# Optimization experiments

Measured on AMD Instinct MI355X. Metric: run time of the kernel, lower is better.

## Reference

```python
import jax, jax.numpy as jnp
import numpy as np

D_MODEL = 512
N_HEAD = 8
D_HEAD = D_MODEL // N_HEAD
EPS = 1e-6


def setup_inputs() -> dict:
    key = jax.random.key(0)
    ks = jax.random.split(key, 11)
    b, s, d = 4, 8192, D_MODEL
    scale = 1.0 / np.sqrt(d)
    inp = {
        "q": jax.random.normal(ks[0], (b, s, d), jnp.float32),
        "k": jax.random.normal(ks[1], (b, s, d), jnp.float32),
        "v": jax.random.normal(ks[2], (b, s, d), jnp.float32),
        "Wq": jax.random.normal(ks[3], (d, d), jnp.float32) * scale,
        "bq": jax.random.normal(ks[4], (d,), jnp.float32) * 0.01,
        "Wk": jax.random.normal(ks[5], (d, d), jnp.float32) * scale,
        "bk": jax.random.normal(ks[6], (d,), jnp.float32) * 0.01,
        "Wv": jax.random.normal(ks[7], (d, d), jnp.float32) * scale,
        "bv": jax.random.normal(ks[8], (d,), jnp.float32) * 0.01,
        "Wo": jax.random.normal(ks[9], (d, d), jnp.float32) * scale,
        "bo": jax.random.normal(ks[10], (d,), jnp.float32) * 0.01,
    }
    return inp


def reference(q, k, v, Wq, bq, Wk, bk, Wv, bv, Wo, bo):
    b, s, d = q.shape
    # torch nn.Linear: x @ W.T + b
    feat = lambda x, W, bias: jax.nn.elu(
        (x @ W.T + bias).reshape(b, s, N_HEAD, D_HEAD)) + 1.0
    queries = feat(q, Wq, bq)                      # [b,s,h,dh]
    keys = feat(k, Wk, bk)                         # [b,s,h,dh]
    values = (v @ Wv.T + bv).reshape(b, s, N_HEAD, D_HEAD)
    # full-sequence KV summary state
    k_v = jnp.einsum('bshd,bshm->bhdm', keys, values)   # [b,h,dh,dh]
    z = keys.sum(axis=1, keepdims=True)                 # [b,1,h,dh]
    num = jnp.einsum('bshd,bhdm->bshm', queries, k_v)   # [b,s,h,dh]
    den = jnp.sum(queries * z, axis=-1)                 # [b,s,h] (broadcast over s)
    out = num / (den[..., None] + EPS)
    out = out.reshape(b, s, d)
    return (out @ Wo.T + bo, k_v, z)
```

## Files before the change

### kernel.cpp

```cpp
#include <hip/hip_runtime.h>
#include <hip/hip_bf16.h>
#include <stdint.h>

typedef __bf16 bf16x8 __attribute__((ext_vector_type(8)));
typedef float f32x4 __attribute__((ext_vector_type(4)));

#define S_LEN 8192
#define BATCH 4
#define DMODEL 512
#define NHEAD 8
#define DHEAD 64
#define MROWS (BATCH * S_LEN)
#define OUT0_ELEMS (MROWS * DMODEL)
#define KV_ELEMS (BATCH * NHEAD * DHEAD * DHEAD)
#define Z_ELEMS (BATCH * NHEAD * DHEAD)

__device__ __forceinline__ uint16_t f2bf(float f) {
    uint32_t u = __float_as_uint(f);
    u = (u + 0x7fffu + ((u >> 16) & 1u)) >> 16;
    return (uint16_t)u;
}
__device__ __forceinline__ uint32_t pack2(float a, float b) {
    union { __hip_bfloat162 h; uint32_t u; } cv;
    cv.h = __float22bfloat162_rn(make_float2(a, b));
    return cv.u;
}
__device__ __forceinline__ void gload_lds16(const void* g, void* l) {
    __builtin_amdgcn_global_load_lds(
        (const __attribute__((address_space(1))) void*)g,
        (__attribute__((address_space(3))) void*)l, 16, 0, 0);
}

__global__ void wconv_kernel(const float* __restrict__ w0, const float* __restrict__ w1,
                             const float* __restrict__ w2, const float* __restrict__ w3,
                             uint16_t* __restrict__ dst) {
    const float* src = (blockIdx.y == 0) ? w0 : (blockIdx.y == 1) ? w1
                       : (blockIdx.y == 2) ? w2 : w3;
    uint16_t* d = dst + (size_t)blockIdx.y * (DMODEL * DMODEL);
    int i = (blockIdx.x * 256 + threadIdx.x) * 4;
    float4 v = *(const float4*)(src + i);
    uint2 o;
    o.x = pack2(v.x, v.y);
    o.y = pack2(v.z, v.w);
    *(uint2*)(d + i) = o;
}

template<bool A_F32, bool ELU1, bool OUT_F32, bool OUT_TRANS>
__global__ __launch_bounds__(256, 3)
void gemm_kernel(const void* __restrict__ Ap, const uint16_t* __restrict__ Wb,
                 const float* __restrict__ bias, void* __restrict__ Cp)
{
    __shared__ uint4 smem4[2048];
    uint16_t* sA0 = (uint16_t*)smem4;
    uint16_t* sB0 = sA0 + 4096;
    uint16_t* sA1 = sB0 + 4096;
    uint16_t* sB1 = sA1 + 4096;
    const int tid = threadIdx.x;
    const int lane = tid & 63, w = tid >> 6;
    const int quad = lane >> 4, l15 = lane & 15;
    const int m_blk = blockIdx.x * 128, n_blk = blockIdx.y * 128;
    const int g0 = w * 2;

    f32x4 acc[4][4];
#pragma unroll
    for (int mi = 0; mi < 4; ++mi)
#pragma unroll
        for (int ni = 0; ni < 4; ++ni) acc[mi][ni] = (f32x4){0.f, 0.f, 0.f, 0.f};

    const int ar = tid >> 1;
    const int ah = tid & 1;
    const float* arow_base = A_F32 ? ((const float*)Ap + (size_t)(m_blk + ar) * 512 + ah * 16)
                                   : nullptr;
    const uint16_t* Ab = (const uint16_t*)Ap;

    auto loadA = [&](int t, float4* r) {
        const float* p = arow_base + t * 32;
        r[0] = *(const float4*)(p);
        r[1] = *(const float4*)(p + 4);
        r[2] = *(const float4*)(p + 8);
        r[3] = *(const float4*)(p + 12);
    };
    auto packA = [&](uint16_t* sA, const float4* r) {
        uint16_t* base = sA + (((ar >> 4) * 4 + ah * 2) * 16 + (ar & 15)) * 8;
        *(uint4*)base = make_uint4(pack2(r[0].x, r[0].y), pack2(r[0].z, r[0].w),
                                   pack2(r[1].x, r[1].y), pack2(r[1].z, r[1].w));
        *(uint4*)(base + 128) = make_uint4(pack2(r[2].x, r[2].y), pack2(r[2].z, r[2].w),
                                           pack2(r[3].x, r[3].y), pack2(r[3].z, r[3].w));
    };
    auto stageB = [&](uint16_t* sB, int t) {
        const int k0 = t * 32;
        gload_lds16(Wb + (size_t)(n_blk + g0 * 16 + l15) * 512 + k0 + quad * 8,
                    sB + g0 * 512);
        gload_lds16(Wb + (size_t)(n_blk + (g0 + 1) * 16 + l15) * 512 + k0 + quad * 8,
                    sB + (g0 + 1) * 512);
    };
    auto stageA16 = [&](uint16_t* sA, int t) {
        const int k0 = t * 32;
        gload_lds16(Ab + (size_t)(m_blk + g0 * 16 + l15) * 512 + k0 + quad * 8,
                    sA + g0 * 512);
        gload_lds16(Ab + (size_t)(m_blk + (g0 + 1) * 16 + l15) * 512 + k0 + quad * 8,
                    sA + (g0 + 1) * 512);
    };
    auto compute = [&](const uint16_t* sA, const uint16_t* sB) {
        bf16x8 afr[4], bfr[4];
#pragma unroll
        for (int mi = 0; mi < 4; ++mi)
            afr[mi] = *(const bf16x8*)(sA + (((w & 1) * 4 + mi) * 64 + lane) * 8);
#pragma unroll
        for (int ni = 0; ni < 4; ++ni)
            bfr[ni] = *(const bf16x8*)(sB + (((w >> 1) * 4 + ni) * 64 + lane) * 8);
#pragma unroll
        for (int mi = 0; mi < 4; ++mi)
#pragma unroll
            for (int ni = 0; ni < 4; ++ni)
                acc[mi][ni] = __builtin_amdgcn_mfma_f32_16x16x32_bf16(
                    afr[mi], bfr[ni], acc[mi][ni], 0, 0, 0);
    };

    float4 rX[4], rY[4];
    if (A_F32) loadA(0, rY);
    stageB(sB0, 0);
    if (A_F32) { loadA(1, rX); packA(sA0, rY); }
    else       stageA16(sA0, 0);
    __syncthreads();

    for (int p = 0; p < 8; ++p) {
        const int t0 = 2 * p;
        if (A_F32 && p < 7) loadA(t0 + 2, rY);
        stageB(sB1, t0 + 1);
        if (A_F32) packA(sA1, rX);
        else       stageA16(sA1, t0 + 1);
        compute(sA0, sB0);
        __syncthreads();
        if (p < 7) {
            if (A_F32) loadA(t0 + 3, rX);
            stageB(sB0, t0 + 2);
            if (A_F32) packA(sA0, rY);
            else       stageA16(sA0, t0 + 2);
        }
        compute(sA1, sB1);
        __syncthreads();
    }

    const int mw = (w & 1) * 64, nw = (w >> 1) * 64;
    float bias4[4];
#pragma unroll
    for (int ni = 0; ni < 4; ++ni) bias4[ni] = bias[n_blk + nw + ni * 16 + l15];

    if (OUT_TRANS) {
        uint16_t* t = (uint16_t*)smem4 + w * 2560;
        uint16_t* C = (uint16_t*)Cp;
        const int bb = m_blk >> 13;
        const int s_base = (m_blk & 8191) + mw;
#pragma unroll
        for (int p = 0; p < 2; ++p) {
#pragma unroll
            for (int mi2 = 0; mi2 < 2; ++mi2) {
                const int mi = p * 2 + mi2;
#pragma unroll
                for (int ni = 0; ni < 4; ++ni)
#pragma unroll
                    for (int r = 0; r < 4; ++r) {
                        float val = acc[mi][ni][r] + bias4[ni];
                        if (ELU1) val = (val > 0.f) ? (val + 1.f) : __expf(val);
                        t[(ni * 16 + l15) * 40 + mi2 * 16 + quad * 4 + r] = f2bf(val);
                    }
            }
#pragma unroll
            for (int it = 0; it < 4; ++it) {
                const int idx = it * 64 + lane;
                const int col = idx >> 2, sg = idx & 3;
                uint4 vv = *(const uint4*)(t + col * 40 + sg * 8);
                *(uint4*)(C + ((size_t)(bb * 512) + n_blk + nw + col) * 8192
                            + s_base + p * 32 + sg * 8) = vv;
            }
        }
    } else if (OUT_F32) {
        float* t = (float*)(smem4 + w * 256);
        float* C = (float*)Cp;
#pragma unroll
        for (int mi = 0; mi < 4; ++mi) {
#pragma unroll
            for (int ni = 0; ni < 4; ++ni)
#pragma unroll
                for (int r = 0; r < 4; ++r) {
                    float val = acc[mi][ni][r] + bias4[ni];
                    if (ELU1) val = (val > 0.f) ? (val + 1.f) : __expf(val);
                    t[(quad * 4 + r) * 64 + ni * 16 + l15] = val;
                }
#pragma unroll
            for (int c = 0; c < 4; ++c) {
                const int idx = c * 64 + lane;
                const int row = idx >> 4, colc = (idx & 15) * 4;
                float4 vv = *(const float4*)(t + row * 64 + colc);
                *(float4*)(C + (size_t)(m_blk + mw + mi * 16 + row) * 512
                             + n_blk + nw + colc) = vv;
            }
        }
    } else {
        uint16_t* t = (uint16_t*)(smem4 + w * 128);
        uint16_t* C = (uint16_t*)Cp;
#pragma unroll
        for (int mi = 0; mi < 4; ++mi) {
#pragma unroll
            for (int ni = 0; ni < 4; ++ni)
#pragma unroll
                for (int r = 0; r < 4; ++r) {
                    float val = acc[mi][ni][r] + bias4[ni];
                    if (ELU1) val = (val > 0.f) ? (val + 1.f) : __expf(val);
                    t[(quad * 4 + r) * 64 + ni * 16 + l15] = f2bf(val);
                }
#pragma unroll
            for (int c = 0; c < 2; ++c) {
                const int idx = c * 64 + lane;
                const int row = idx >> 3, colc = (idx & 7) * 8;
                uint4 vv = *(const uint4*)(t + row * 64 + colc);
                *(uint4*)(C + (size_t)(m_blk + mw + mi * 16 + row) * 512
                            + n_blk + nw + colc) = vv;
            }
        }
    }
}

__global__ __launch_bounds__(256, 4)
void kv_kernel(const uint16_t* __restrict__ KT, const uint16_t* __restrict__ VT,
               float* __restrict__ kvz)
{
    const int tid = threadIdx.x;
    const int lane = tid & 63, w = tid >> 6;
    const int quad = lane >> 4, l15 = lane & 15;
    const int bh = blockIdx.y, b = bh >> 3, h = bh & 7;
    const int dh2 = w & 1, mh2 = w >> 1;
    const int S0 = blockIdx.x * 512;

    const uint16_t* Ka[2];
    const uint16_t* Va[2];
#pragma unroll
    for (int i = 0; i < 2; ++i) {
        Ka[i] = KT + (size_t)(b * 512 + h * 64 + dh2 * 32 + i * 16 + l15) * 8192 + S0 + quad * 8;
        Va[i] = VT + (size_t)(b * 512 + h * 64 + mh2 * 32 + i * 16 + l15) * 8192 + S0 + quad * 8;
    }

    f32x4 acc[2][2], accz[2];
#pragma unroll
    for (int mi = 0; mi < 2; ++mi) {
        accz[mi] = (f32x4){0.f, 0.f, 0.f, 0.f};
#pragma unroll
        for (int ni = 0; ni < 2; ++ni) acc[mi][ni] = (f32x4){0.f, 0.f, 0.f, 0.f};
    }
    bf16x8 ones;
#pragma unroll
    for (int j = 0; j < 8; ++j) ones[j] = (__bf16)1.0f;

    uint4 ka[2], va[2];
#pragma unroll
    for (int i = 0; i < 2; ++i) {
        ka[i] = *(const uint4*)(Ka[i]);
        va[i] = *(const uint4*)(Va[i]);
    }

#pragma unroll
    for (int it = 0; it < 16; ++it) {
        uint4 kn[2], vn[2];
        if (it < 15) {
#pragma unroll
            for (int i = 0; i < 2; ++i) {
                kn[i] = *(const uint4*)(Ka[i] + (it + 1) * 32);
                vn[i] = *(const uint4*)(Va[i] + (it + 1) * 32);
            }
        }
        bf16x8 afr[2], bfr[2];
#pragma unroll
        for (int i = 0; i < 2; ++i) {
            union { uint4 u; bf16x8 v; } ca, cb;
            ca.u = ka[i]; afr[i] = ca.v;
            cb.u = va[i]; bfr[i] = cb.v;
        }
#pragma unroll
        for (int mi = 0; mi < 2; ++mi)
#pragma unroll
            for (int ni = 0; ni < 2; ++ni)
                acc[mi][ni] = __builtin_amdgcn_mfma_f32_16x16x32_bf16(
                    afr[mi], bfr[ni], acc[mi][ni], 0, 0, 0);
        if (mh2 == 0) {
#pragma unroll
            for (int mi = 0; mi < 2; ++mi)
                accz[mi] = __builtin_amdgcn_mfma_f32_16x16x32_bf16(
                    afr[mi], ones, accz[mi], 0, 0, 0);
        }
        if (it < 15) {
#pragma unroll
            for (int i = 0; i < 2; ++i) { ka[i] = kn[i]; va[i] = vn[i]; }
        }
    }
    float* kvp = kvz + (size_t)bh * 4096;
#pragma unroll
    for (int mi = 0; mi < 2; ++mi)
#pragma unroll
        for (int ni = 0; ni < 2; ++ni)
#pragma unroll
            for (int r = 0; r < 4; ++r)
                atomicAdd(kvp + (dh2 * 32 + mi * 16 + quad * 4 + r) * 64
                              + mh2 * 32 + ni * 16 + l15, acc[mi][ni][r]);
    if (mh2 == 0 && l15 == 0) {
#pragma unroll
        for (int mi = 0; mi < 2; ++mi)
#pragma unroll
            for (int r = 0; r < 4; ++r)
                atomicAdd(kvz + KV_ELEMS + bh * 64 + dh2 * 32 + mi * 16 + quad * 4 + r,
                          accz[mi][r]);
    }
}

__global__ void kvf_kernel(const float* __restrict__ kvz, uint16_t* __restrict__ KVf) {
    const int bh = blockIdx.x;
    const int tid = threadIdx.x;
    for (int e = tid; e < 5120; e += 256) {
        const int j = e & 7, c = e >> 3;
        const int l15c = c & 15, quadc = (c >> 4) & 3, kkc = (c >> 6) & 1, ng = c >> 7;
        const int n = ng * 16 + l15c;
        const int d = kkc * 32 + quadc * 8 + j;
        float val = (n < 64) ? kvz[(size_t)bh * 4096 + d * 64 + n]
                  : ((n == 64) ? kvz[KV_ELEMS + bh * 64 + d] : 0.f);
        KVf[(size_t)bh * 5120 + e] = f2bf(val);
    }
}

__global__ __launch_bounds__(256, 4)
void attn_kernel(const uint16_t* __restrict__ Qb, const uint16_t* __restrict__ KVf,
                 uint16_t* __restrict__ Yb)
{
    __shared__ uint4 smem4[1152];
    uint16_t* sB = (uint16_t*)smem4;
    uint16_t* sEp = (uint16_t*)(smem4 + 640);
    const int bh = blockIdx.y;
    const int b = bh >> 3, h = bh & 7;
    const int tid = threadIdx.x;
    const int lane = tid & 63, w = tid >> 6, quad = lane >> 4, l15 = lane & 15;

    const uint16_t* src = KVf + (size_t)bh * 5120;
    gload_lds16(src + (size_t)tid * 8,         sB + (w * 64) * 8);
    gload_lds16(src + (size_t)(256 + tid) * 8, sB + ((256 + w * 64)) * 8);
    if (tid < 128)
        gload_lds16(src + (size_t)(512 + tid) * 8, sB + ((512 + w * 64)) * 8);
    __syncthreads();

    f32x4 acc[2][5];
#pragma unroll
    for (int mi = 0; mi < 2; ++mi)
#pragma unroll
        for (int ni = 0; ni < 5; ++ni) acc[mi][ni] = (f32x4){0.f, 0.f, 0.f, 0.f};
    const int row0 = blockIdx.x * 128 + w * 32;
#pragma unroll
    for (int kk = 0; kk < 2; ++kk) {
        bf16x8 afr[2];
#pragma unroll
        for (int mi = 0; mi < 2; ++mi) {
            const size_t ga = (size_t)(b * S_LEN + row0 + mi * 16 + l15) * DMODEL
                              + h * DHEAD + kk * 32 + quad * 8;
            afr[mi] = *(const bf16x8*)(Qb + ga);
        }
#pragma unroll
        for (int ni = 0; ni < 5; ++ni) {
            bf16x8 bfr = *(const bf16x8*)(sB + ((ni * 2 + kk) * 64 + lane) * 8);
            acc[0][ni] = __builtin_amdgcn_mfma_f32_16x16x32_bf16(afr[0], bfr, acc[0][ni], 0, 0, 0);
            acc[1][ni] = __builtin_amdgcn_mfma_f32_16x16x32_bf16(afr[1], bfr, acc[1][ni], 0, 0, 0);
        }
    }
    uint16_t* t = sEp + w * 1024;
#pragma unroll
    for (int mi = 0; mi < 2; ++mi) {
        float rden[4];
#pragma unroll
        for (int r = 0; r < 4; ++r) {
            const float den = __shfl(acc[mi][4][r], lane & 48, 64);
            rden[r] = 1.0f / (den + 1e-6f);
        }
#pragma unroll
        for (int ni = 0; ni < 4; ++ni)
#pragma unroll
            for (int r = 0; r < 4; ++r)
                t[(quad * 4 + r) * 64 + ni * 16 + l15] = f2bf(acc[mi][ni][r] * rden[r]);
#pragma unroll
        for (int c = 0; c < 2; ++c) {
            const int idx = c * 64 + lane;
            const int row = idx >> 3, colc = (idx & 7) * 8;
            uint4 vv = *(const uint4*)(t + row * 64 + colc);
            *(uint4*)(Yb + (size_t)(b * S_LEN + row0 + mi * 16 + row) * 512
                        + h * DHEAD + colc) = vv;
        }
    }
}

extern "C" void kernel_launch(void* const* d_in, const int* in_sizes, int n_in,
                              void* d_out, int out_size, void* d_ws, size_t ws_size,
                              hipStream_t stream)
{
    const float* q  = (const float*)d_in[0];
    const float* k  = (const float*)d_in[1];
    const float* v  = (const float*)d_in[2];
    const float* Wq = (const float*)d_in[3];
    const float* bq = (const float*)d_in[4];
    const float* Wk = (const float*)d_in[5];
    const float* bk = (const float*)d_in[6];
    const float* Wv = (const float*)d_in[7];
    const float* bv = (const float*)d_in[8];
    const float* Wo = (const float*)d_in[9];
    const float* bo = (const float*)d_in[10];

    uint16_t* Qb = (uint16_t*)d_ws;
    uint16_t* KT = Qb + OUT0_ELEMS;
    uint16_t* VT = KT + OUT0_ELEMS;
    uint16_t* Wb = VT + OUT0_ELEMS;
    uint16_t* KVf = VT;
    uint16_t* Yb = KT;

    float* out0 = (float*)d_out;
    float* kvz  = out0 + OUT0_ELEMS;

    hipMemsetAsync(kvz, 0, (KV_ELEMS + Z_ELEMS) * sizeof(float), stream);
    wconv_kernel<<<dim3(256, 4), 256, 0, stream>>>(Wq, Wk, Wv, Wo, Wb);
    gemm_kernel<true, true,  false, false><<<dim3(256, 4), 256, 0, stream>>>(q, Wb,              bq, Qb);
    gemm_kernel<true, true,  false, true ><<<dim3(256, 4), 256, 0, stream>>>(k, Wb + 262144,     bk, KT);
    gemm_kernel<true, false, false, true ><<<dim3(256, 4), 256, 0, stream>>>(v, Wb + 2 * 262144, bv, VT);
    kv_kernel<<<dim3(16, 32), 256, 0, stream>>>(KT, VT, kvz);
    kvf_kernel<<<dim3(32), 256, 0, stream>>>(kvz, KVf);
    attn_kernel<<<dim3(64, 32), 256, 0, stream>>>(Qb, KVf, Yb);
    gemm_kernel<false, false, true, false><<<dim3(256, 4), 256, 0, stream>>>(Yb, Wb + 3 * 262144, bo, out0);
}
```

Baseline: 430.6 us.

## Merge Q/K/V projections into one launch and pipeline GEMM loads with vmcnt waits

After: 377.7 us. 12.3% less time.

```diff
diff --git a/kernel.cpp b/kernel.cpp
--- a/kernel.cpp
+++ b/kernel.cpp
@@ -14,6 +14,15 @@
 #define OUT0_ELEMS (MROWS * DMODEL)
 #define KV_ELEMS (BATCH * NHEAD * DHEAD * DHEAD)
 #define Z_ELEMS (BATCH * NHEAD * DHEAD)
+
+#define WAITV6() asm volatile("s_waitcnt vmcnt(6)" ::: "memory")
+#define WAITV4() asm volatile("s_waitcnt vmcnt(4)" ::: "memory")
+#define WAITV2() asm volatile("s_waitcnt vmcnt(2)" ::: "memory")
+#define WAITV0() asm volatile("s_waitcnt vmcnt(0)" ::: "memory")
+#define WAITL0() asm volatile("s_waitcnt lgkmcnt(0)" ::: "memory")
+#define BARRIER() do { asm volatile("" ::: "memory"); \
+                       __builtin_amdgcn_s_barrier(); \
+                       asm volatile("" ::: "memory"); } while (0)
 
 __device__ __forceinline__ uint16_t f2bf(float f) {
     uint32_t u = __float_as_uint(f);
@@ -45,21 +54,27 @@
     *(uint2*)(d + i) = o;
 }
 
-template<bool A_F32, bool ELU1, bool OUT_F32, bool OUT_TRANS>
 __global__ __launch_bounds__(256, 3)
-void gemm_kernel(const void* __restrict__ Ap, const uint16_t* __restrict__ Wb,
-                 const float* __restrict__ bias, void* __restrict__ Cp)
+void gemm_qkv_kernel(const float* __restrict__ qp, const float* __restrict__ kp,
+                     const float* __restrict__ vp, const uint16_t* __restrict__ Wb,
+                     const float* __restrict__ bq, const float* __restrict__ bk,
+                     const float* __restrict__ bv,
+                     uint16_t* __restrict__ Qb, uint16_t* __restrict__ KT,
+                     uint16_t* __restrict__ VT)
 {
     __shared__ uint4 smem4[2048];
-    uint16_t* sA0 = (uint16_t*)smem4;
-    uint16_t* sB0 = sA0 + 4096;
-    uint16_t* sA1 = sB0 + 4096;
-    uint16_t* sB1 = sA1 + 4096;
+    uint16_t* sAb[2] = {(uint16_t*)smem4, (uint16_t*)smem4 + 8192};
+    uint16_t* sBb[2] = {(uint16_t*)smem4 + 4096, (uint16_t*)smem4 + 12288};
     const int tid = threadIdx.x;
     const int lane = tid & 63, w = tid >> 6;
     const int quad = lane >> 4, l15 = lane & 15;
-    const int m_blk = blockIdx.x * 128, n_blk = blockIdx.y * 128;
+    const int which = blockIdx.y >> 2;
+    const int m_blk = blockIdx.x * 128, n_blk = (blockIdx.y & 3) * 128;
     const int g0 = w * 2;
+
+    const float* Af = (which == 0) ? qp : (which == 1) ? kp : vp;
+    const float* bias = (which == 0) ? bq : (which == 1) ? bk : bv;
+    const uint16_t* Wm = Wb + (size_t)which * 262144;
 
     f32x4 acc[4][4];
 #pragma unroll
@@ -69,9 +84,7 @@
 
     const int ar = tid >> 1;
     const int ah = tid & 1;
-    const float* arow_base = A_F32 ? ((const float*)Ap + (size_t)(m_blk + ar) * 512 + ah * 16)
-                                   : nullptr;
-    const uint16_t* Ab = (const uint16_t*)Ap;
+    const float* arow_base = Af + (size_t)(m_blk + ar) * 512 + ah * 16;
 
     auto loadA = [&](int t, float4* r) {
         const float* p = arow_base + t * 32;
@@ -89,17 +102,10 @@
     };
     auto stageB = [&](uint16_t* sB, int t) {
         const int k0 = t * 32;
-        gload_lds16(Wb + (size_t)(n_blk + g0 * 16 + l15) * 512 + k0 + quad * 8,
+        gload_lds16(Wm + (size_t)(n_blk + g0 * 16 + l15) * 512 + k0 + quad * 8,
                     sB + g0 * 512);
-        gload_lds16(Wb + (size_t)(n_blk + (g0 + 1) * 16 + l15) * 512 + k0 + quad * 8,
+        gload_lds16(Wm + (size_t)(n_blk + (g0 + 1) * 16 + l15) * 512 + k0 + quad * 8,
                     sB + (g0 + 1) * 512);
-    };
-    auto stageA16 = [&](uint16_t* sA, int t) {
-        const int k0 = t * 32;
-        gload_lds16(Ab + (size_t)(m_blk + g0 * 16 + l15) * 512 + k0 + quad * 8,
-                    sA + g0 * 512);
-        gload_lds16(Ab + (size_t)(m_blk + (g0 + 1) * 16 + l15) * 512 + k0 + quad * 8,
-                    sA + (g0 + 1) * 512);
     };
     auto compute = [&](const uint16_t* sA, const uint16_t* sB) {
         bf16x8 afr[4], bfr[4];
@@ -117,39 +123,59 @@
                     afr[mi], bfr[ni], acc[mi][ni], 0, 0, 0);
     };
 
-    float4 rX[4], rY[4];
-    if (A_F32) loadA(0, rY);
-    stageB(sB0, 0);
-    if (A_F32) { loadA(1, rX); packA(sA0, rY); }
-    else       stageA16(sA0, 0);
+    float4 rA[2][4];
+    stageB(sBb[0], 0);
+    loadA(0, rA[0]);
+    packA(sAb[0], rA[0]);
+    loadA(1, rA[1]);
+
+#pragma unroll
+    for (int t = 0; t < 16; ++t) {
+        const int cur = t & 1, nxt = cur ^ 1;
+        if (t < 15) stageB(sBb[nxt], t + 1);
+        if (t < 14) loadA(t + 2, rA[cur]);
+        if (t < 15) packA(sAb[nxt], rA[nxt]);
+        if (t < 14)      { WAITV6(); }
+        else if (t == 14){ WAITV2(); }
+        else             { WAITV0(); }
+        WAITL0();
+        BARRIER();
+        compute(sAb[cur], sBb[cur]);
+        BARRIER();
+    }
     __syncthreads();
 
-    for (int p = 0; p < 8; ++p) {
-        const int t0 = 2 * p;
-        if (A_F32 && p < 7) loadA(t0 + 2, rY);
-        stageB(sB1, t0 + 1);
-        if (A_F32) packA(sA1, rX);
-        else       stageA16(sA1, t0 + 1);
-        compute(sA0, sB0);
-        __syncthreads();
-        if (p < 7) {
-            if (A_F32) loadA(t0 + 3, rX);
-            stageB(sB0, t0 + 2);
-            if (A_F32) packA(sA0, rY);
-            else       stageA16(sA0, t0 + 2);
-        }
-        compute(sA1, sB1);
-        __syncthreads();
-    }
-
     const int mw = (w & 1) * 64, nw = (w >> 1) * 64;
+    const bool elu = (which != 2);
     float bias4[4];
 #pragma unroll
     for (int ni = 0; ni < 4; ++ni) bias4[ni] = bias[n_blk + nw + ni * 16 + l15];
 
-    if (OUT_TRANS) {
+    if (which == 0) {
+        uint16_t* t = (uint16_t*)smem4 + w * 2048;
+        uint16_t* C = Qb;
+#pragma unroll
+        for (int mi = 0; mi < 4; ++mi) {
+#pragma unroll
+            for (int ni = 0; ni < 4; ++ni)
+#pragma unroll
+                for (int r = 0; r < 4; ++r) {
+                    float val = acc[mi][ni][r] + bias4[ni];
+                    val = (val > 0.f) ? (val + 1.f) : __expf(val);
+                    t[(quad * 4 + r) * 64 + ni * 16 + l15] = f2bf(val);
+                }
+#pragma unroll
+            for (int c = 0; c < 2; ++c) {
+                const int idx = c * 64 + lane;
+                const int row = idx >> 3, colc = (idx & 7) * 8;
+                uint4 vv = *(const uint4*)(t + row * 64 + colc);
+                *(uint4*)(C + (size_t)(m_blk + mw + mi * 16 + row) * 512
+                            + n_blk + nw + colc) = vv;
+            }
+        }
+    } else {
         uint16_t* t = (uint16_t*)smem4 + w * 2560;
-        uint16_t* C = (uint16_t*)Cp;
+        uint16_t* C = (which == 1) ? KT : VT;
         const int bb = m_blk >> 13;
         const int s_base = (m_blk & 8191) + mw;
 #pragma unroll
@@ -162,7 +188,7 @@
 #pragma unroll
                     for (int r = 0; r < 4; ++r) {
                         float val = acc[mi][ni][r] + bias4[ni];
-                        if (ELU1) val = (val > 0.f) ? (val + 1.f) : __expf(val);
+                        if (elu) val = (val > 0.f) ? (val + 1.f) : __expf(val);
                         t[(ni * 16 + l15) * 40 + mi2 * 16 + quad * 4 + r] = f2bf(val);
                     }
             }
@@ -175,49 +201,91 @@
                             + s_base + p * 32 + sg * 8) = vv;
             }
         }
-    } else if (OUT_F32) {
-        float* t = (float*)(smem4 + w * 256);
-        float* C = (float*)Cp;
-#pragma unroll
-        for (int mi = 0; mi < 4; ++mi) {
+    }
+}
+
+__global__ __launch_bounds__(256, 3)
+void gemm_out_kernel(const uint16_t* __restrict__ Ab, const uint16_t* __restrict__ Wm,
+                     const float* __restrict__ bias, float* __restrict__ C)
+{
+    __shared__ uint4 smem4[2048];
+    uint16_t* sAb[2] = {(uint16_t*)smem4, (uint16_t*)smem4 + 8192};
+    uint16_t* sBb[2] = {(uint16_t*)smem4 + 4096, (uint16_t*)smem4 + 12288};
+    const int tid = threadIdx.x;
+    const int lane = tid & 63, w = tid >> 6;
+    const int quad = lane >> 4, l15 = lane & 15;
+    const int m_blk = blockIdx.x * 128, n_blk = blockIdx.y * 128;
+    const int g0 = w * 2;
+
+    f32x4 acc[4][4];
+#pragma unroll
+    for (int mi = 0; mi < 4; ++mi)
+#pragma unroll
+        for (int ni = 0; ni < 4; ++ni) acc[mi][ni] = (f32x4){0.f, 0.f, 0.f, 0.f};
+
+    auto stageA = [&](uint16_t* sA, int t) {
+        const int k0 = t * 32;
+        gload_lds16(Ab + (size_t)(m_blk + g0 * 16 + l15) * 512 + k0 + quad * 8,
+                    sA + g0 * 512);
+        gload_lds16(Ab + (size_t)(m_blk + (g0 + 1) * 16 + l15) * 512 + k0 + quad * 8,
+                    sA + (g0 + 1) * 512);
+    };
+    auto stageB = [&](uint16_t* sB, int t) {
+        const int k0 = t * 32;
+        gload_lds16(Wm + (size_t)(n_blk + g0 * 16 + l15) * 512 + k0 + quad * 8,
+                    sB + g0 * 512);
+        gload_lds16(Wm + (size_t)(n_blk + (g0 + 1) * 16 + l15) * 512 + k0 + quad * 8,
+                    sB + (g0 + 1) * 512);
+    };
+    auto compute = [&](const uint16_t* sA, const uint16_t* sB) {
+        bf16x8 afr[4], bfr[4];
+#pragma unroll
+        for (int mi = 0; mi < 4; ++mi)
+            afr[mi] = *(const bf16x8*)(sA + (((w & 1) * 4 + mi) * 64 + lane) * 8);
+#pragma unroll
+        for (int ni = 0; ni < 4; ++ni)
+            bfr[ni] = *(const bf16x8*)(sB + (((w >> 1) * 4 + ni) * 64 + lane) * 8);
+#pragma unroll
+        for (int mi = 0; mi < 4; ++mi)
 #pragma unroll
             for (int ni = 0; ni < 4; ++ni)
-#pragma unroll
-                for (int r = 0; r < 4; ++r) {
-                    float val = acc[mi][ni][r] + bias4[ni];
-                    if (ELU1) val = (val > 0.f) ? (val + 1.f) : __expf(val);
-                    t[(quad * 4 + r) * 64 + ni * 16 + l15] = val;
-                }
-#pragma unroll
-            for (int c = 0; c < 4; ++c) {
-                const int idx = c * 64 + lane;
-                const int row = idx >> 4, colc = (idx & 15) * 4;
-                float4 vv = *(const float4*)(t + row * 64 + colc);
-                *(float4*)(C + (size_t)(m_blk + mw + mi * 16 + row) * 512
-                             + n_blk + nw + colc) = vv;
-            }
-        }
-    } else {
-        uint16_t* t = (uint16_t*)(smem4 + w * 128);
-        uint16_t* C = (uint16_t*)Cp;
-#pragma unroll
-        for (int mi = 0; mi < 4; ++mi) {
-#pragma unroll
-            for (int ni = 0; ni < 4; ++ni)
-#pragma unroll
-                for (int r = 0; r < 4; ++r) {
-                    float val = acc[mi][ni][r] + bias4[ni];
-                    if (ELU1) val = (val > 0.f) ? (val + 1.f) : __expf(val);
-                    t[(quad * 4 + r) * 64 + ni * 16 + l15] = f2bf(val);
-                }
-#pragma unroll
-            for (int c = 0; c < 2; ++c) {
-                const int idx = c * 64 + lane;
-                const int row = idx >> 3, colc = (idx & 7) * 8;
-                uint4 vv = *(const uint4*)(t + row * 64 + colc);
-                *(uint4*)(C + (size_t)(m_blk + mw + mi * 16 + row) * 512
-                            + n_blk + nw + colc) = vv;
-            }
+                acc[mi][ni] = __builtin_amdgcn_mfma_f32_16x16x32_bf16(
+                    afr[mi], bfr[ni], acc[mi][ni], 0, 0, 0);
+    };
+
+    stageA(sAb[0], 0);
+    stageB(sBb[0], 0);
+#pragma unroll
+    for (int t = 0; t < 16; ++t) {
+        const int cur = t & 1, nxt = cur ^ 1;
+        if (t < 15) { stageA(sAb[nxt], t + 1); stageB(sBb[nxt], t + 1); }
+        if (t < 15) { WAITV4(); } else { WAITV0(); }
+        BARRIER();
+        compute(sAb[cur], sBb[cur]);
+        BARRIER();
+    }
+    __syncthreads();
+
+    const int mw = (w & 1) * 64, nw = (w >> 1) * 64;
+    float bias4[4];
+#pragma unroll
+    for (int ni = 0; ni < 4; ++ni) bias4[ni] = bias[n_blk + nw + ni * 16 + l15];
+
+    float* t = (float*)(smem4 + w * 256);
+#pragma unroll
+    for (int mi = 0; mi < 4; ++mi) {
+#pragma unroll
+        for (int ni = 0; ni < 4; ++ni)
+#pragma unroll
+            for (int r = 0; r < 4; ++r)
+                t[(quad * 4 + r) * 64 + ni * 16 + l15] = acc[mi][ni][r] + bias4[ni];
+#pragma unroll
+        for (int c = 0; c < 4; ++c) {
+            const int idx = c * 64 + lane;
+            const int row = idx >> 4, colc = (idx & 15) * 4;
+            float4 vv = *(const float4*)(t + row * 64 + colc);
+            *(float4*)(C + (size_t)(m_blk + mw + mi * 16 + row) * 512
+                         + n_blk + nw + colc) = vv;
         }
     }
 }
@@ -420,11 +488,10 @@
 
     hipMemsetAsync(kvz, 0, (KV_ELEMS + Z_ELEMS) * sizeof(float), stream);
     wconv_kernel<<<dim3(256, 4), 256, 0, stream>>>(Wq, Wk, Wv, Wo, Wb);
-    gemm_kernel<true, true,  false, false><<<dim3(256, 4), 256, 0, stream>>>(q, Wb,              bq, Qb);
-    gemm_kernel<true, true,  false, true ><<<dim3(256, 4), 256, 0, stream>>>(k, Wb + 262144,     bk, KT);
-    gemm_kernel<true, false, false, true ><<<dim3(256, 4), 256, 0, stream>>>(v, Wb + 2 * 262144, bv, VT);
+    gemm_qkv_kernel<<<dim3(256, 12), 256, 0, stream>>>(q, k, v, Wb, bq, bk, bv,
+                                                       Qb, KT, VT);
     kv_kernel<<<dim3(16, 32), 256, 0, stream>>>(KT, VT, kvz);
     kvf_kernel<<<dim3(32), 256, 0, stream>>>(kvz, KVf);
     attn_kernel<<<dim3(64, 32), 256, 0, stream>>>(Qb, KVf, Yb);
-    gemm_kernel<false, false, true, false><<<dim3(256, 4), 256, 0, stream>>>(Yb, Wb + 3 * 262144, bo, out0);
-}
+    gemm_out_kernel<<<dim3(256, 4), 256, 0, stream>>>(Yb, Wb + 3 * 262144, bo, out0);
+}
```
